# Optimization experiments

Hardware: AMD Instinct MI355X
Metric: run time of the kernel (lower is better)

## Reference

```python
import jax, jax.numpy as jnp
import numpy as np

CURIOSITY_COEF = 0.1
EPS = 1e-8


def _stratified_norm(r, m, eps):
    """Min-max normalize r within mask m per group row. r, m: [B, G]."""
    cnt = jnp.sum(m, axis=1, keepdims=True)                      # [B, 1]
    rmin = jnp.min(jnp.where(m, r, jnp.inf), axis=1, keepdims=True)
    rmax = jnp.max(jnp.where(m, r, -jnp.inf), axis=1, keepdims=True)
    # Sanitize empty strata (cnt == 0) so no inf/nan propagates; those lanes
    # are discarded by the outer correctness select anyway.
    rmin = jnp.where(cnt > 0, rmin, 0.0)
    rmax = jnp.where(cnt > 0, rmax, 0.0)
    n = (r - rmin) / (rmax - rmin + eps)
    # Singleton stratum gets 0.5, matching the torch reference.
    return jnp.where(cnt == 1, 0.5, n)


def setup_inputs() -> dict:
    key = jax.random.key(0)
    k1, k2 = jax.random.split(key)
    N = 33554432  # B*G = 2_097_152 * 16
    rewards = jax.random.normal(k1, (N,), dtype=jnp.float32)
    correctness = jax.random.bernoulli(k2, 0.5, (N,))  # bool
    return {"rewards": rewards, "correctness": correctness, "group_size": 16}


def reference(rewards, correctness, group_size):
    B = rewards.shape[0] // group_size
    r = rewards.reshape(B, group_size)
    c = correctness.reshape(B, group_size)
    n_correct = _stratified_norm(r, c, EPS)
    n_incorrect = _stratified_norm(r, ~c, EPS)
    normalized = jnp.where(c, n_correct, n_incorrect).reshape(-1)  # [B*G] in [0,1]
    signed = jnp.where(correctness,
                       CURIOSITY_COEF * normalized,
                       -CURIOSITY_COEF * normalized)
    return signed
```

## Files before the change

### kernel.cpp

```cpp
#include <hip/hip_runtime.h>

#define CURIOSITY_COEF 0.1f
#define EPS_F 1e-8f

typedef float f32x4 __attribute__((ext_vector_type(4)));
typedef int   i32x4 __attribute__((ext_vector_type(4)));

__global__ __launch_bounds__(256) void srnd_kernel(
    const f32x4* __restrict__ r4,
    const i32x4* __restrict__ c4,
    f32x4*       __restrict__ o4,
    int Q)
{
    int q = blockIdx.x * blockDim.x + threadIdx.x;
    if (q >= Q) return;

    f32x4 rr = r4[q];
    i32x4 cc = c4[q];
    float rv[4] = {rr.x, rr.y, rr.z, rr.w};
    int   cv[4] = {cc.x, cc.y, cc.z, cc.w};

    float minC =  INFINITY, maxC = -INFINITY;
    float minI =  INFINITY, maxI = -INFINITY;
    int   cntC = 0;
    #pragma unroll
    for (int i = 0; i < 4; ++i) {
        bool  c = (cv[i] != 0);
        float v = rv[i];
        minC = fminf(minC, c ? v :  INFINITY);
        maxC = fmaxf(maxC, c ? v : -INFINITY);
        minI = fminf(minI, c ?  INFINITY : v);
        maxI = fmaxf(maxI, c ? -INFINITY : v);
        cntC += c ? 1 : 0;
    }

    #pragma unroll
    for (int m = 1; m <= 2; m <<= 1) {
        minC = fminf(minC, __shfl_xor(minC, m));
        maxC = fmaxf(maxC, __shfl_xor(maxC, m));
        minI = fminf(minI, __shfl_xor(minI, m));
        maxI = fmaxf(maxI, __shfl_xor(maxI, m));
        cntC +=            __shfl_xor(cntC, m);
    }
    int cntI = 16 - cntC;

    float invC = 1.0f / (maxC - minC + EPS_F);
    float invI = 1.0f / (maxI - minI + EPS_F);

    f32x4 ov;
    #pragma unroll
    for (int i = 0; i < 4; ++i) {
        bool  c = (cv[i] != 0);
        float n;
        if (c)
            n = (cntC == 1) ? 0.5f : (rv[i] - minC) * invC;
        else
            n = (cntI == 1) ? 0.5f : (rv[i] - minI) * invI;
        ov[i] = c ? (CURIOSITY_COEF * n) : (-CURIOSITY_COEF * n);
    }

    __builtin_nontemporal_store(ov, &o4[q]);
}

extern "C" void kernel_launch(void* const* d_in, const int* in_sizes, int n_in,
                              void* d_out, int out_size, void* d_ws, size_t ws_size,
                              hipStream_t stream) {
    const float* rewards = (const float*)d_in[0];
    const int*   corr    = (const int*)d_in[1];
    float*       out     = (float*)d_out;

    int N = in_sizes[0];
    int Q = N / 4;

    const int threads = 256;
    const int blocks  = (Q + threads - 1) / threads;
    srnd_kernel<<<blocks, threads, 0, stream>>>(
        reinterpret_cast<const f32x4*>(rewards),
        reinterpret_cast<const i32x4*>(corr),
        reinterpret_cast<f32x4*>(out), Q);
}
```

Before: 59.28 us.

## Batch four vector loads per thread and use DPP quad reductions

Each thread now processes four strided float4/int4 chunks, issuing all loads up front to raise memory-level parallelism, with the grid shrunk to match. Quad-lane min/max/count reductions use DPP moves instead of shuffles, and max is computed as a negated min. The division becomes a hardware reciprocal, and the output is folded into one FMA per element. This trades slightly lower reciprocal precision and higher register use for fewer instructions and more in-flight loads.

New measurement: 65.89 us. +11.1%, slower.

```diff
diff --git a/kernel.cpp b/kernel.cpp
--- a/kernel.cpp
+++ b/kernel.cpp
@@ -2,9 +2,23 @@
 
 #define CURIOSITY_COEF 0.1f
 #define EPS_F 1e-8f
+#define ITERS 4
 
 typedef float f32x4 __attribute__((ext_vector_type(4)));
 typedef int   i32x4 __attribute__((ext_vector_type(4)));
+
+__device__ __forceinline__ float fqxor1(float x) {
+    return __int_as_float(__builtin_amdgcn_mov_dpp(__float_as_int(x), 0xB1, 0xF, 0xF, true));
+}
+__device__ __forceinline__ float fqxor2(float x) {
+    return __int_as_float(__builtin_amdgcn_mov_dpp(__float_as_int(x), 0x4E, 0xF, 0xF, true));
+}
+__device__ __forceinline__ int iqxor1(int x) {
+    return __builtin_amdgcn_mov_dpp(x, 0xB1, 0xF, 0xF, true);
+}
+__device__ __forceinline__ int iqxor2(int x) {
+    return __builtin_amdgcn_mov_dpp(x, 0x4E, 0xF, 0xF, true);
+}
 
 __global__ __launch_bounds__(256) void srnd_kernel(
     const f32x4* __restrict__ r4,
@@ -12,54 +26,75 @@
     f32x4*       __restrict__ o4,
     int Q)
 {
-    int q = blockIdx.x * blockDim.x + threadIdx.x;
-    if (q >= Q) return;
+    int tid = blockIdx.x * blockDim.x + threadIdx.x;
+    int S   = gridDim.x * blockDim.x;
 
-    f32x4 rr = r4[q];
-    i32x4 cc = c4[q];
-    float rv[4] = {rr.x, rr.y, rr.z, rr.w};
-    int   cv[4] = {cc.x, cc.y, cc.z, cc.w};
-
-    float minC =  INFINITY, maxC = -INFINITY;
-    float minI =  INFINITY, maxI = -INFINITY;
-    int   cntC = 0;
+    f32x4 rr[ITERS];
+    i32x4 cc[ITERS];
     #pragma unroll
-    for (int i = 0; i < 4; ++i) {
-        bool  c = (cv[i] != 0);
-        float v = rv[i];
-        minC = fminf(minC, c ? v :  INFINITY);
-        maxC = fmaxf(maxC, c ? v : -INFINITY);
-        minI = fminf(minI, c ?  INFINITY : v);
-        maxI = fmaxf(maxI, c ? -INFINITY : v);
-        cntC += c ? 1 : 0;
+    for (int i = 0; i < ITERS; ++i) {
+        int q = tid + i * S;
+        if (q < Q) { rr[i] = r4[q]; cc[i] = c4[q]; }
     }
 
     #pragma unroll
-    for (int m = 1; m <= 2; m <<= 1) {
-        minC = fminf(minC, __shfl_xor(minC, m));
-        maxC = fmaxf(maxC, __shfl_xor(maxC, m));
-        minI = fminf(minI, __shfl_xor(minI, m));
-        maxI = fmaxf(maxI, __shfl_xor(maxI, m));
-        cntC +=            __shfl_xor(cntC, m);
+    for (int i = 0; i < ITERS; ++i) {
+        int q = tid + i * S;
+        if (q >= Q) continue;
+
+        float v[4]  = {rr[i].x, rr[i].y, rr[i].z, rr[i].w};
+        int   cm[4] = {cc[i].x, cc[i].y, cc[i].z, cc[i].w};
+
+        float minC = INFINITY, nmxC = INFINITY;
+        float minI = INFINITY, nmxI = INFINITY;
+        int   cnt  = 0;
+        #pragma unroll
+        for (int e = 0; e < 4; ++e) {
+            bool  c = (cm[e] != 0);
+            float x = v[e];
+            minC = fminf(minC, c ?  x : INFINITY);
+            nmxC = fminf(nmxC, c ? -x : INFINITY);
+            minI = fminf(minI, c ? INFINITY :  x);
+            nmxI = fminf(nmxI, c ? INFINITY : -x);
+            cnt += c ? 1 : 0;
+        }
+
+        minC = fminf(minC, fqxor1(minC));
+        nmxC = fminf(nmxC, fqxor1(nmxC));
+        minI = fminf(minI, fqxor1(minI));
+        nmxI = fminf(nmxI, fqxor1(nmxI));
+        cnt += iqxor1(cnt);
+        minC = fminf(minC, fqxor2(minC));
+        nmxC = fminf(nmxC, fqxor2(nmxC));
+        minI = fminf(minI, fqxor2(minI));
+        nmxI = fminf(nmxI, fqxor2(nmxI));
+        cnt += iqxor2(cnt);
+
+        int cntC = cnt;
+        int cntI = 16 - cnt;
+
+        float dC   = -nmxC - minC + EPS_F;
+        float dI   = -nmxI - minI + EPS_F;
+        float invC = __builtin_amdgcn_rcpf(dC);
+        float invI = __builtin_amdgcn_rcpf(dI);
+        float aC =  CURIOSITY_COEF * invC;
+        float bC = -aC * minC;
+        float aI = -CURIOSITY_COEF * invI;
+        float bI = -aI * minI;
+        if (cntC == 1) { aC = 0.0f; bC =  0.05f; }
+        if (cntI == 1) { aI = 0.0f; bI = -0.05f; }
+
+        f32x4 ov;
+        #pragma unroll
+        for (int e = 0; e < 4; ++e) {
+            bool  c = (cm[e] != 0);
+            float a = c ? aC : aI;
+            float b = c ? bC : bI;
+            ov[e] = fmaf(v[e], a, b);
+        }
+
+        __builtin_nontemporal_store(ov, &o4[q]);
     }
-    int cntI = 16 - cntC;
-
-    float invC = 1.0f / (maxC - minC + EPS_F);
-    float invI = 1.0f / (maxI - minI + EPS_F);
-
-    f32x4 ov;
-    #pragma unroll
-    for (int i = 0; i < 4; ++i) {
-        bool  c = (cv[i] != 0);
-        float n;
-        if (c)
-            n = (cntC == 1) ? 0.5f : (rv[i] - minC) * invC;
-        else
-            n = (cntI == 1) ? 0.5f : (rv[i] - minI) * invI;
-        ov[i] = c ? (CURIOSITY_COEF * n) : (-CURIOSITY_COEF * n);
-    }
-
-    __builtin_nontemporal_store(ov, &o4[q]);
 }
 
 extern "C" void kernel_launch(void* const* d_in, const int* in_sizes, int n_in,
@@ -73,7 +108,7 @@
     int Q = N / 4;
 
     const int threads = 256;
-    const int blocks  = (Q + threads - 1) / threads;
+    const int blocks  = (Q + threads * ITERS - 1) / (threads * ITERS);
     srnd_kernel<<<blocks, threads, 0, stream>>>(
         reinterpret_cast<const f32x4*>(rewards),
         reinterpret_cast<const i32x4*>(corr),
```
